# Kernel tuning notes

Measured on AMD Instinct MI355X. Metric: run time of the kernel, lower is better.

Reference implementation:

```python
import jax, jax.numpy as jnp
import numpy as np

S, N, K = 8, 2048, 64          # snapshots, atoms, max neighbors (sum of max_num_neighs)
L = 20.0                        # periodic box length
R_CS, R_C = 6.0, 12.0           # smooth cutoff radii
M2 = 16                         # dim_sub_net


def _mlp(x, params, resnet=False):
    # DenseChainNet: Linear -> relu per layer; resnet skip when dims match or double (DeepMD style)
    for W, b in params:
        y = jax.nn.relu(x @ W + b)
        if resnet and y.shape[-1] == x.shape[-1]:
            y = y + x
        elif resnet and y.shape[-1] == 2 * x.shape[-1]:
            y = y + jnp.concatenate([x, x], axis=-1)
        x = y
    return x


def setup_inputs() -> dict:
    ks = jax.random.split(jax.random.key(0), 14)
    inputs = jax.random.uniform(ks[0], (S, N, 3), jnp.float32) * L
    input_types = jax.random.randint(ks[1], (S, N), 0, 2)
    nl = jax.random.randint(ks[2], (S, N, K), 0, N)
    neigh_list = jnp.where(jax.random.uniform(ks[3], (S, N, K)) < 0.2, -1, nl)  # -1 = padded neighbor

    def w(k, i, o):
        return jax.random.normal(k, (i, o), jnp.float32) / np.float32(np.sqrt(i))

    return {
        'inputs': inputs,
        'input_types': input_types,
        'neigh_list': neigh_list,
        'length': jnp.array([L, L, L], jnp.float32),
        # embed_species (species_dim [2,16,32])
        'ew0': w(ks[4], 2, 16), 'eb0': jnp.zeros((16,), jnp.float32),
        'ew1': w(ks[5], 16, 32), 'eb1': jnp.zeros((32,), jnp.float32),
        # fit_species (species_fit [32,32,31])
        'fw0': w(ks[6], 32, 32), 'fb0': jnp.zeros((32,), jnp.float32),
        'fw1': w(ks[7], 32, 31), 'fb1': jnp.zeros((31,), jnp.float32),
        # embed_net (descript_dim [32,64,128], resnet=True)
        'gw0': w(ks[8], 32, 64), 'gb0': jnp.zeros((64,), jnp.float32),
        'gw1': w(ks[9], 64, 128), 'gb1': jnp.zeros((128,), jnp.float32),
    }


def reference(inputs, input_types, neigh_list, length,
              ew0, eb0, ew1, eb1, fw0, fb0, fw1, fb1, gw0, gb0, gw1, gb1):
    mask = neigh_list == -1                                   # [S,N,K]
    idx = jnp.where(mask, 0, neigh_list)

    # ---- gen_coordinates_smooth: neighbor gather + min-image + smooth cutoff ----
    neigh_pos = jax.vmap(lambda p, i: p[i])(inputs, idx)      # [S,N,K,3]
    diff = neigh_pos - inputs[:, :, None, :]
    diff = diff - length * jnp.round(diff / length)           # minimum image convention
    rsq = jnp.sum(diff * diff, axis=-1)
    r = jnp.sqrt(jnp.where(rsq > 0, rsq, 1.0))                # safe sqrt (self/padded pairs)
    inv = 1.0 / r
    u = (r - R_CS) / (R_C - R_CS)
    sw = jnp.where(r < R_CS, inv,
                   jnp.where(r < R_C, inv * (0.5 * jnp.cos(jnp.pi * u) + 0.5), 0.0))
    valid = (~mask) & (rsq > 0)
    s_ij = jnp.where(valid, sw, 0.0)                          # [S,N,K]  s(r)
    r_ij = diff * (s_ij / r)[..., None]                       # [S,N,K,3] s(r)*x/r

    # ---- SpeciesModule: pair-type embedding (symmetrized) ----
    neigh_types = jax.vmap(lambda t, i: t[i])(input_types, idx)           # [S,N,K]
    center = jnp.broadcast_to(input_types[:, :, None], (S, N, K))
    pairs = jnp.stack([center, neigh_types], axis=-1).astype(jnp.float32).reshape(-1, 2)
    emb = [(ew0, eb0), (ew1, eb1)]
    t = _mlp(pairs, emb) + _mlp(pairs[:, ::-1], emb)
    td = _mlp(t, [(fw0, fb0), (fw1, fb1)]).reshape(S, N, K, -1)           # [S,N,K,31]
    td = jnp.where(mask[..., None], 0.0, td)

    # ---- embedding net + descriptor contraction ----
    s_tilde = jnp.concatenate([td, s_ij[..., None]], axis=-1)             # [S,N,K,32]
    G = _mlp(s_tilde.reshape(S * N * K, -1), [(gw0, gb0), (gw1, gb1)],
             resnet=True).reshape(S, N, K, -1)                            # [S,N,K,128]
    r_tilde = jnp.concatenate([s_ij[..., None], r_ij], axis=-1)           # [S,N,K,4]
    G2 = G[..., :M2]
    R = jnp.einsum('snkd,snkm->sndm', r_tilde, G2)                        # [S,N,4,16]
    R1 = jnp.einsum('snkd,sndm->snkm', r_tilde, R)                        # [S,N,K,16]
    D = jnp.einsum('snke,snkm->snem', G, R1)                              # [S,N,128,16]
    return D
```

## Files before the change

kernel.cpp:

```cpp
#include <hip/hip_runtime.h>
#include <math.h>

#define S_DIM 8
#define N_DIM 2048
#define K_DIM 64
#define APW 4
#define ST_ST 40
#define ST_H1 72

typedef __attribute__((ext_vector_type(8))) short bf16x8;
typedef __attribute__((ext_vector_type(4))) float f32x4;
typedef __attribute__((ext_vector_type(4))) int   i32x4;

__device__ __forceinline__ unsigned asu(float x) {
    union { float f; unsigned u; } v; v.f = x; return v.u;
}
__device__ __forceinline__ unsigned short f2bf(float x) {
    unsigned u = asu(x);
    return (unsigned short)((u + 0x7FFFu + ((u >> 16) & 1u)) >> 16);
}
__device__ __forceinline__ float bf2f(unsigned short h) {
    union { unsigned u; float f; } v; v.u = ((unsigned)h) << 16; return v.f;
}
__device__ __forceinline__ unsigned rne_pk(float x, float y) {
    unsigned ux = asu(x), uy = asu(y);
    return ((ux + 0x7FFFu + ((ux >> 16) & 1u)) >> 16) |
           ((uy + 0x7FFFu + ((uy >> 16) & 1u)) & 0xFFFF0000u);
}
__device__ __forceinline__ unsigned trn_pk(float x, float y) {
    return (asu(x) >> 16) | (asu(y) & 0xFFFF0000u);
}
__device__ __forceinline__ void lds_fence() {
    asm volatile("s_waitcnt lgkmcnt(0)" ::: "memory");
    __builtin_amdgcn_sched_barrier(0);
}
__device__ __forceinline__ f32x4 mfma_k16(unsigned a0, unsigned a1,
                                          unsigned b0, unsigned b1, f32x4 c) {
    union { i32x4 i; bf16x8 b; } ua, ub;
    ua.i = (i32x4){(int)a0, (int)a1, 0, 0};
    ub.i = (i32x4){(int)b0, (int)b1, 0, 0};
    return __builtin_amdgcn_mfma_f32_16x16x32_bf16(ua.b, ub.b, c, 0, 0, 0);
}

__global__ __launch_bounds__(256) void prep_kernel(
        const float* __restrict__ ew0, const float* __restrict__ eb0,
        const float* __restrict__ ew1, const float* __restrict__ eb1,
        const float* __restrict__ fw0, const float* __restrict__ fb0,
        const float* __restrict__ fw1, const float* __restrict__ fb1,
        const float* __restrict__ gw0, const float* __restrict__ gw1,
        unsigned* __restrict__ td_pk,
        unsigned short* __restrict__ w0t, unsigned short* __restrict__ w1t) {
    __shared__ float l_ew0[32], l_eb0[16], l_ew1[512], l_eb1[32];
    __shared__ float l_fw0[1024], l_fb0[32], l_fw1[992], l_fb1[31];
    __shared__ float l_h[4][2][16];
    __shared__ float l_tv[4][32];
    __shared__ float l_f1[4][32];
    __shared__ float l_td[4][32];

    const int tid = threadIdx.x;
    if (tid < 32) l_ew0[tid] = ew0[tid];
    if (tid < 16) l_eb0[tid] = eb0[tid];
    for (int i = tid; i < 512; i += 256) l_ew1[i] = ew1[i];
    if (tid < 32) l_eb1[tid] = eb1[tid];
    for (int i = tid; i < 1024; i += 256) l_fw0[i] = fw0[i];
    if (tid < 32) l_fb0[tid] = fb0[tid];
    for (int i = tid; i < 992; i += 256) l_fw1[i] = fw1[i];
    if (tid < 31) l_fb1[tid] = fb1[tid];
    __syncthreads();

    if (tid < 128) {
        const int p = tid >> 5, ord = (tid >> 4) & 1, j = tid & 15;
        const float c = (float)(p >> 1), t = (float)(p & 1);
        const float x0 = ord ? t : c;
        const float x1 = ord ? c : t;
        l_h[p][ord][j] = fmaxf(x0 * l_ew0[j] + x1 * l_ew0[16 + j] + l_eb0[j], 0.f);
    }
    __syncthreads();
    if (tid < 128) {
        const int p = tid >> 5, j = tid & 31;
        float acc = 0.f;
#pragma unroll
        for (int ord = 0; ord < 2; ord++) {
            float v = l_eb1[j];
#pragma unroll
            for (int i = 0; i < 16; i++) v += l_h[p][ord][i] * l_ew1[i * 32 + j];
            acc += fmaxf(v, 0.f);
        }
        l_tv[p][j] = acc;
    }
    __syncthreads();
    if (tid < 128) {
        const int p = tid >> 5, j = tid & 31;
        float v = l_fb0[j];
#pragma unroll
        for (int i = 0; i < 32; i++) v += l_tv[p][i] * l_fw0[i * 32 + j];
        l_f1[p][j] = fmaxf(v, 0.f);
    }
    __syncthreads();
    if (tid < 128) {
        const int p = tid >> 5, j = tid & 31;
        if (j < 31) {
            float v = l_fb1[j];
#pragma unroll
            for (int i = 0; i < 32; i++) v += l_f1[p][i] * l_fw1[i * 31 + j];
            l_td[p][j] = fmaxf(v, 0.f);
        } else {
            l_td[p][31] = 0.f;
        }
    }
    __syncthreads();
    if (tid < 64) {
        const int p = tid >> 4, i = tid & 15;
        const unsigned lo = f2bf(l_td[p][2 * i]);
        const unsigned hi = (i == 15) ? 0u : (unsigned)f2bf(l_td[p][2 * i + 1]);
        td_pk[tid] = lo | (hi << 16);
    }

    for (int idx = tid; idx < 2048; idx += 256) {
        const int j = idx >> 5, i = idx & 31;
        w0t[idx] = f2bf(gw0[i * 64 + j]);
    }
    for (int idx = tid; idx < 8192; idx += 256) {
        const int e = idx >> 6, j = idx & 63;
        w1t[idx] = f2bf(gw1[j * 128 + e]);
    }
}

__global__ __launch_bounds__(64, 2) void descr_mfma(
    const float* __restrict__ inputs, const int* __restrict__ input_types,
    const int* __restrict__ neigh_list, const float* __restrict__ length,
    const float* __restrict__ gb0, const float* __restrict__ gb1,
    const unsigned* __restrict__ td_pk, const unsigned short* __restrict__ w0t,
    const unsigned short* __restrict__ w1t, float* __restrict__ out)
{
    __shared__ __align__(16) unsigned short s_st[64 * ST_ST];
    __shared__ __align__(16) unsigned short s_h1[2][16 * ST_H1];
    __shared__ __align__(16) float s_rtT[4 * 68];
    __shared__ unsigned s_tdpk[64];
    float* s_A = (float*)s_st;

    const int lane = threadIdx.x;
    const int l15 = lane & 15;
    const int q = lane >> 4;
    const int abase = blockIdx.x * APW;
    const int sidx = abase >> 11;

    bf16x8 w0f[4];
#pragma unroll
    for (int nt = 0; nt < 4; nt++)
        w0f[nt] = *(const bf16x8*)&w0t[(nt * 16 + l15) * 32 + q * 8];
    bf16x8 w1f[8][2];
#pragma unroll
    for (int et = 0; et < 8; et++) {
        w1f[et][0] = *(const bf16x8*)&w1t[(et * 16 + l15) * 64 + q * 8];
        w1f[et][1] = *(const bf16x8*)&w1t[(et * 16 + l15) * 64 + 32 + q * 8];
    }
    float b0f[4], b1f[8];
#pragma unroll
    for (int jt = 0; jt < 4; jt++) b0f[jt] = gb0[jt * 16 + l15];
#pragma unroll
    for (int et = 0; et < 8; et++) b1f[et] = gb1[et * 16 + l15];
    s_tdpk[lane] = td_pk[lane];
    const float Lx = length[0], Ly = length[1], Lz = length[2];
    const float iLx = 1.f / Lx, iLy = 1.f / Ly, iLz = 1.f / Lz;
    const f32x4 zf = {0.f, 0.f, 0.f, 0.f};

    int   cnb  = neigh_list[abase * K_DIM + lane];
    float ccx  = inputs[abase * 3 + 0];
    float ccy  = inputs[abase * 3 + 1];
    float ccz  = inputs[abase * 3 + 2];
    int   cct  = input_types[abase];
    int   cidx0 = cnb < 0 ? 0 : cnb;
    float cpx  = inputs[(sidx * N_DIM + cidx0) * 3 + 0];
    float cpy  = inputs[(sidx * N_DIM + cidx0) * 3 + 1];
    float cpz  = inputs[(sidx * N_DIM + cidx0) * 3 + 2];
    int   cntp = input_types[sidx * N_DIM + cidx0];

    for (int aa = 0; aa < APW; aa++) {
        const int atom = abase + aa;
        const bool pf = (aa + 1 < APW);

        int nnb = 0, nct = 0; float ncx = 0.f, ncy = 0.f, ncz = 0.f;
        if (pf) {
            nnb = neigh_list[(atom + 1) * K_DIM + lane];
            ncx = inputs[(atom + 1) * 3 + 0];
            ncy = inputs[(atom + 1) * 3 + 1];
            ncz = inputs[(atom + 1) * 3 + 2];
            nct = input_types[atom + 1];
        }

        lds_fence();

        {
            const bool msk = cnb < 0;
            float dx = cpx - ccx;
            float dy = cpy - ccy;
            float dz = cpz - ccz;
            dx -= Lx * rintf(dx * iLx);
            dy -= Ly * rintf(dy * iLy);
            dz -= Lz * rintf(dz * iLz);
            const float rsq = dx * dx + dy * dy + dz * dz;
            const float r = sqrtf(rsq > 0.f ? rsq : 1.f);
            const float inv = 1.f / r;
            float sw;
            if (r < 6.f) sw = inv;
            else if (r < 12.f) {
                const float u = (r - 6.f) * (1.f / 6.f);
                sw = inv * (0.5f * __cosf(3.14159265358979323846f * u) + 0.5f);
            } else sw = 0.f;
            const bool valid = (!msk) && (rsq > 0.f);
            const float sij = valid ? sw : 0.f;
            const float f = sij * inv;
            s_rtT[0 * 68 + lane] = sij;
            s_rtT[1 * 68 + lane] = dx * f;
            s_rtT[2 * 68 + lane] = dy * f;
            s_rtT[3 * 68 + lane] = dz * f;

            const unsigned* tdr = &s_tdpk[(cct * 2 + cntp) * 16];
            const unsigned zmask = msk ? 0u : 0xFFFFFFFFu;
            unsigned* strow = (unsigned*)&s_st[lane * ST_ST];
#pragma unroll
            for (int i = 0; i < 15; i++) strow[i] = tdr[i] & zmask;
            strow[15] = (tdr[15] & zmask & 0xFFFFu) | (((unsigned)f2bf(sij)) << 16);
            strow[16] = 0; strow[17] = 0; strow[18] = 0; strow[19] = 0;
        }
        lds_fence();

        unsigned rtp[4][2];
#pragma unroll
        for (int a = 0; a < 4; a++) {
            const f32x4 rv = *(const f32x4*)&s_rtT[(l15 & 3) * 68 + a * 16 + q * 4];
            rtp[a][0] = rne_pk(rv[0], rv[1]);
            rtp[a][1] = rne_pk(rv[2], rv[3]);
        }

        int nidx = 0, nntp = 0; float npx = 0.f, npy = 0.f, npz = 0.f;
        f32x4 Bj[4] = {zf, zf, zf, zf};
        f32x4 AT[8] = {zf, zf, zf, zf, zf, zf, zf, zf};

#pragma unroll
        for (int mt = 0; mt < 4; mt++) {
            unsigned short* h1c = s_h1[mt & 1];
            const bf16x8 afr = *(const bf16x8*)&s_st[(mt * 16 + l15) * ST_ST + q * 8];
            f32x4 c1[4];
#pragma unroll
            for (int jt = 0; jt < 4; jt++)
                c1[jt] = __builtin_amdgcn_mfma_f32_16x16x32_bf16(afr, w0f[jt], zf, 0, 0, 0);
#pragma unroll
            for (int jt = 0; jt < 4; jt++) {
                float hv[4];
#pragma unroll
                for (int reg = 0; reg < 4; reg++) {
                    const int k = mt * 16 + q * 4 + reg;
                    const float rres = bf2f(s_st[k * ST_ST + (jt & 1) * 16 + l15]);
                    hv[reg] = fmaxf(c1[jt][reg] + b0f[jt], 0.f) + rres;
                    h1c[(q * 4 + reg) * ST_H1 + jt * 16 + l15] = f2bf(hv[reg]);
                }
                Bj[jt] = mfma_k16(rtp[mt][0], rtp[mt][1],
                                  trn_pk(hv[0], hv[1]), trn_pk(hv[2], hv[3]), Bj[jt]);
            }
            if (mt == 0 && pf) {
                nidx = nnb < 0 ? 0 : nnb;
                const int nbase = (sidx * N_DIM + nidx) * 3;
                npx = inputs[nbase + 0];
                npy = inputs[nbase + 1];
                npz = inputs[nbase + 2];
                nntp = input_types[sidx * N_DIM + nidx];
            }
            lds_fence();

            const bf16x8 a0 = *(const bf16x8*)&h1c[l15 * ST_H1 + q * 8];
            const bf16x8 a1 = *(const bf16x8*)&h1c[l15 * ST_H1 + 32 + q * 8];
#pragma unroll
            for (int et = 0; et < 8; et++) {
                f32x4 c2 = __builtin_amdgcn_mfma_f32_16x16x32_bf16(a0, w1f[et][0], zf, 0, 0, 0);
                c2 = __builtin_amdgcn_mfma_f32_16x16x32_bf16(a1, w1f[et][1], c2, 0, 0, 0);
                const float g0 = fmaxf(c2[0] + b1f[et], 0.f);
                const float g1 = fmaxf(c2[1] + b1f[et], 0.f);
                const float g2 = fmaxf(c2[2] + b1f[et], 0.f);
                const float g3 = fmaxf(c2[3] + b1f[et], 0.f);
                AT[et] = mfma_k16(rtp[mt][0], rtp[mt][1],
                                  trn_pk(g0, g1), trn_pk(g2, g3), AT[et]);
            }
        }

        if (lane < 16) {
#pragma unroll
            for (int et = 0; et < 8; et++) {
                const f32x4 v = AT[et] + Bj[et & 3];
                *(f32x4*)&s_A[(et * 16 + lane) * 4] = v;
            }
        }
        lds_fence();

        {
            const int m0 = (lane & 3) * 4;
            const int er = lane >> 2;
            f32x4 Am[4];
#pragma unroll
            for (int t = 0; t < 4; t++) Am[t] = *(const f32x4*)&s_A[(m0 + t) * 4];
            float* op = out + (size_t)atom * 2048;
#pragma unroll
            for (int g = 0; g < 8; g++) {
                const int e = g * 16 + er;
                const f32x4 Ae = *(const f32x4*)&s_A[e * 4];
                f32x4 o;
                o[0] = Ae[0]*Am[0][0] + Ae[1]*Am[0][1] + Ae[2]*Am[0][2] + Ae[3]*Am[0][3];
                o[1] = Ae[0]*Am[1][0] + Ae[1]*Am[1][1] + Ae[2]*Am[1][2] + Ae[3]*Am[1][3];
                o[2] = Ae[0]*Am[2][0] + Ae[1]*Am[2][1] + Ae[2]*Am[2][2] + Ae[3]*Am[2][3];
                o[3] = Ae[0]*Am[3][0] + Ae[1]*Am[3][1] + Ae[2]*Am[3][2] + Ae[3]*Am[3][3];
                *(f32x4*)&op[e * 16 + m0] = o;
            }
        }

        cnb = nnb; ccx = ncx; ccy = ncy; ccz = ncz; cct = nct;
        cpx = npx; cpy = npy; cpz = npz; cntp = nntp;
    }
}

extern "C" void kernel_launch(void* const* d_in, const int* in_sizes, int n_in,
                              void* d_out, int out_size, void* d_ws, size_t ws_size,
                              hipStream_t stream) {
    (void)in_sizes; (void)n_in; (void)out_size; (void)ws_size;
    const float* inputs      = (const float*)d_in[0];
    const int*   input_types = (const int*)d_in[1];
    const int*   neigh_list  = (const int*)d_in[2];
    const float* length      = (const float*)d_in[3];
    const float* ew0 = (const float*)d_in[4];
    const float* eb0 = (const float*)d_in[5];
    const float* ew1 = (const float*)d_in[6];
    const float* eb1 = (const float*)d_in[7];
    const float* fw0 = (const float*)d_in[8];
    const float* fb0 = (const float*)d_in[9];
    const float* fw1 = (const float*)d_in[10];
    const float* fb1 = (const float*)d_in[11];
    const float* gw0 = (const float*)d_in[12];
    const float* gb0 = (const float*)d_in[13];
    const float* gw1 = (const float*)d_in[14];
    const float* gb1 = (const float*)d_in[15];
    float* out = (float*)d_out;

    unsigned* td_pk = (unsigned*)d_ws;
    unsigned short* w0t = (unsigned short*)((char*)d_ws + 512);
    unsigned short* w1t = (unsigned short*)((char*)d_ws + 512 + 4096);

    hipLaunchKernelGGL(prep_kernel, dim3(1), dim3(256), 0, stream,
                       ew0, eb0, ew1, eb1, fw0, fb0, fw1, fb1, gw0, gw1,
                       td_pk, w0t, w1t);

    const int nblocks = (S_DIM * N_DIM) / APW;
    hipLaunchKernelGGL(descr_mfma, dim3(nblocks), dim3(64), 0, stream,
                       inputs, input_types, neigh_list, length,
                       gb0, gb1, td_pk, w0t, w1t, out);
}
```

Before: 222.5 us.

## Transpose first-layer MFMA and use ds_read_b64_tr_b16 for hidden-layer fragments

Swaps the operands of the first embedding-layer MFMA so each lane holds a neighbor's hidden features, and writes them to LDS as packed 64-bit stores in a new tiled layout. It then uses the transposing ds_read_b64_tr_b16 LDS load to build the B operands for the r_tilde contraction, and reads the second-layer A fragments from the same buffer. Residual values come from vector loads instead of per-element scalar LDS reads, and bias loads are vectorised. The aim is fewer scalar LDS accesses and less repacking. In exchange it relies on the transposing-load semantics being correct, which risks layout mistakes, and it adds an extra wait.

```diff
diff --git a/kernel.cpp b/kernel.cpp
--- a/kernel.cpp
+++ b/kernel.cpp
@@ -6,11 +6,14 @@
 #define K_DIM 64
 #define APW 4
 #define ST_ST 40
-#define ST_H1 72
+#define TQ 144
+#define TJ (4 * TQ)
+#define H1CH (4 * TJ)
 
 typedef __attribute__((ext_vector_type(8))) short bf16x8;
 typedef __attribute__((ext_vector_type(4))) float f32x4;
 typedef __attribute__((ext_vector_type(4))) int   i32x4;
+typedef __attribute__((ext_vector_type(2))) int   i32x2;
 
 __device__ __forceinline__ unsigned asu(float x) {
     union { float f; unsigned u; } v; v.f = x; return v.u;
@@ -19,8 +22,11 @@
     unsigned u = asu(x);
     return (unsigned short)((u + 0x7FFFu + ((u >> 16) & 1u)) >> 16);
 }
-__device__ __forceinline__ float bf2f(unsigned short h) {
-    union { unsigned u; float f; } v; v.u = ((unsigned)h) << 16; return v.f;
+__device__ __forceinline__ float lo16f(int d) {
+    union { unsigned u; float f; } v; v.u = ((unsigned)d) << 16; return v.f;
+}
+__device__ __forceinline__ float hi16f(int d) {
+    union { unsigned u; float f; } v; v.u = ((unsigned)d) & 0xFFFF0000u; return v.f;
 }
 __device__ __forceinline__ unsigned rne_pk(float x, float y) {
     unsigned ux = asu(x), uy = asu(y);
@@ -134,7 +140,7 @@
     const unsigned short* __restrict__ w1t, float* __restrict__ out)
 {
     __shared__ __align__(16) unsigned short s_st[64 * ST_ST];
-    __shared__ __align__(16) unsigned short s_h1[2][16 * ST_H1];
+    __shared__ __align__(16) char s_h1t[2 * H1CH];
     __shared__ __align__(16) float s_rtT[4 * 68];
     __shared__ unsigned s_tdpk[64];
     float* s_A = (float*)s_st;
@@ -155,15 +161,22 @@
         w1f[et][0] = *(const bf16x8*)&w1t[(et * 16 + l15) * 64 + q * 8];
         w1f[et][1] = *(const bf16x8*)&w1t[(et * 16 + l15) * 64 + 32 + q * 8];
     }
-    float b0f[4], b1f[8];
-#pragma unroll
-    for (int jt = 0; jt < 4; jt++) b0f[jt] = gb0[jt * 16 + l15];
+    f32x4 b0v[4];
+#pragma unroll
+    for (int jt = 0; jt < 4; jt++)
+        b0v[jt] = *(const f32x4*)&gb0[jt * 16 + q * 4];
+    float b1f[8];
 #pragma unroll
     for (int et = 0; et < 8; et++) b1f[et] = gb1[et * 16 + l15];
     s_tdpk[lane] = td_pk[lane];
     const float Lx = length[0], Ly = length[1], Lz = length[2];
     const float iLx = 1.f / Lx, iLy = 1.f / Ly, iLz = 1.f / Lz;
     const f32x4 zf = {0.f, 0.f, 0.f, 0.f};
+
+    const unsigned h1u  = (unsigned)(unsigned long long)(const void*)&s_h1t[0];
+    const int wroff = (l15 >> 2) * TQ + (l15 & 3) * 32 + q * 8;
+    const unsigned troff = h1u + (unsigned)(q * TQ + (l15 >> 2) * 32 + (l15 & 3) * 8);
+    const int aoff  = (l15 >> 2) * TQ + (l15 & 3) * 32 + (q & 1) * 16;
 
     int   cnb  = neigh_list[abase * K_DIM + lane];
     float ccx  = inputs[abase * 3 + 0];
@@ -222,7 +235,6 @@
 #pragma unroll
             for (int i = 0; i < 15; i++) strow[i] = tdr[i] & zmask;
             strow[15] = (tdr[15] & zmask & 0xFFFFu) | (((unsigned)f2bf(sij)) << 16);
-            strow[16] = 0; strow[17] = 0; strow[18] = 0; strow[19] = 0;
         }
         lds_fence();
 
@@ -240,24 +252,27 @@
 
 #pragma unroll
         for (int mt = 0; mt < 4; mt++) {
-            unsigned short* h1c = s_h1[mt & 1];
+            const int cb = (mt & 1) * H1CH;
             const bf16x8 afr = *(const bf16x8*)&s_st[(mt * 16 + l15) * ST_ST + q * 8];
+            const i32x2 r0 = *(const i32x2*)&s_st[(mt * 16 + l15) * ST_ST + q * 4];
+            const i32x2 r1 = *(const i32x2*)&s_st[(mt * 16 + l15) * ST_ST + 16 + q * 4];
+
             f32x4 c1[4];
 #pragma unroll
             for (int jt = 0; jt < 4; jt++)
-                c1[jt] = __builtin_amdgcn_mfma_f32_16x16x32_bf16(afr, w0f[jt], zf, 0, 0, 0);
+                c1[jt] = __builtin_amdgcn_mfma_f32_16x16x32_bf16(w0f[jt], afr, zf, 0, 0, 0);
+
 #pragma unroll
             for (int jt = 0; jt < 4; jt++) {
-                float hv[4];
-#pragma unroll
-                for (int reg = 0; reg < 4; reg++) {
-                    const int k = mt * 16 + q * 4 + reg;
-                    const float rres = bf2f(s_st[k * ST_ST + (jt & 1) * 16 + l15]);
-                    hv[reg] = fmaxf(c1[jt][reg] + b0f[jt], 0.f) + rres;
-                    h1c[(q * 4 + reg) * ST_H1 + jt * 16 + l15] = f2bf(hv[reg]);
-                }
-                Bj[jt] = mfma_k16(rtp[mt][0], rtp[mt][1],
-                                  trn_pk(hv[0], hv[1]), trn_pk(hv[2], hv[3]), Bj[jt]);
+                const i32x2 rr = (jt & 1) ? r1 : r0;
+                const float h0 = fmaxf(c1[jt][0] + b0v[jt][0], 0.f) + lo16f(rr[0]);
+                const float h1 = fmaxf(c1[jt][1] + b0v[jt][1], 0.f) + hi16f(rr[0]);
+                const float h2 = fmaxf(c1[jt][2] + b0v[jt][2], 0.f) + lo16f(rr[1]);
+                const float h3 = fmaxf(c1[jt][3] + b0v[jt][3], 0.f) + hi16f(rr[1]);
+                i32x2 pk;
+                pk[0] = (int)rne_pk(h0, h1);
+                pk[1] = (int)rne_pk(h2, h3);
+                *(i32x2*)(s_h1t + cb + wroff + jt * TJ) = pk;
             }
             if (mt == 0 && pf) {
                 nidx = nnb < 0 ? 0 : nnb;
@@ -269,8 +284,23 @@
             }
             lds_fence();
 
-            const bf16x8 a0 = *(const bf16x8*)&h1c[l15 * ST_H1 + q * 8];
-            const bf16x8 a1 = *(const bf16x8*)&h1c[l15 * ST_H1 + 32 + q * 8];
+            i32x2 t0, t1, t2, t3;
+            {
+                const unsigned ta = troff + (unsigned)cb;
+                asm volatile("ds_read_b64_tr_b16 %0, %1" : "=v"(t0) : "v"(ta));
+                asm volatile("ds_read_b64_tr_b16 %0, %1" : "=v"(t1) : "v"(ta + TJ));
+                asm volatile("ds_read_b64_tr_b16 %0, %1" : "=v"(t2) : "v"(ta + 2 * TJ));
+                asm volatile("ds_read_b64_tr_b16 %0, %1" : "=v"(t3) : "v"(ta + 3 * TJ));
+            }
+            asm volatile("s_waitcnt lgkmcnt(0)" ::: "memory");
+            __builtin_amdgcn_sched_barrier(0);
+            Bj[0] = mfma_k16(rtp[mt][0], rtp[mt][1], (unsigned)t0[0], (unsigned)t0[1], Bj[0]);
+            Bj[1] = mfma_k16(rtp[mt][0], rtp[mt][1], (unsigned)t1[0], (unsigned)t1[1], Bj[1]);
+            Bj[2] = mfma_k16(rtp[mt][0], rtp[mt][1], (unsigned)t2[0], (unsigned)t2[1], Bj[2]);
+            Bj[3] = mfma_k16(rtp[mt][0], rtp[mt][1], (unsigned)t3[0], (unsigned)t3[1], Bj[3]);
+
+            const bf16x8 a0 = *(const bf16x8*)(s_h1t + cb + aoff + (q >> 1) * TJ);
+            const bf16x8 a1 = *(const bf16x8*)(s_h1t + cb + aoff + (2 + (q >> 1)) * TJ);
 #pragma unroll
             for (int et = 0; et < 8; et++) {
                 f32x4 c2 = __builtin_amdgcn_mfma_f32_16x16x32_bf16(a0, w1f[et][0], zf, 0, 0, 0);
```

Measured after the change: 218.9 us. No clear change (-1.6%).
